# Performance work log

Hardware: AMD Instinct MI355X
Metric: run time of the kernel (lower is better)

Reference implementation:

```python
import jax, jax.numpy as jnp
import numpy as np

B = 32768
PASSES = 4

# mask layout: (batch, digit, row, col), values in {0,1}

def _to_lines(m, d):
    """Reorder so the last axis enumerates the 9 cells of a line and axis -2 the 9 lines."""
    if d == 'h':
        return m                      # lines = rows, cells = cols
    if d == 'v':
        return jnp.swapaxes(m, 2, 3)  # lines = cols, cells = rows
    b = m.shape[0]                    # lines = 3x3 boxes
    return m.reshape(b, 9, 3, 3, 3, 3).transpose(0, 1, 2, 4, 3, 5).reshape(b, 9, 9, 9)

_from_lines = _to_lines  # all three reorderings are self-inverse


def filter_line(m, d):
    """SudokuFilterHVBox: remove a solved cell's digit from all other cells in its line."""
    l = _to_lines(m, d)
    cnt = l.sum(axis=1, keepdims=True)                 # candidates per cell
    solved = l * (cnt == 1).astype(l.dtype)            # one-hot solved cells
    other = solved.sum(axis=-1, keepdims=True) - solved  # same digit solved elsewhere in line
    out = l * (other == 0).astype(l.dtype)
    return _from_lines(out, d)


def unique_line(m, d):
    """SudokuUniqueHVBox (hidden single): if a digit fits only one cell in a line, fix it."""
    l = _to_lines(m, d)
    cnt_line = l.sum(axis=-1, keepdims=True)           # per-digit count in the line
    hidden = l * (cnt_line == 1).astype(l.dtype)       # lone placements
    has = hidden.sum(axis=1, keepdims=True) > 0        # cell hosts a hidden single
    out = jnp.where(has, hidden, l)
    return _from_lines(out, d)


def doubles_line(m, d):
    """SudokuDigitsDoubles (naked pair): two identical 2-candidate cells in a line
    eliminate those digits from the rest of the line."""
    l = _to_lines(m, d)                                # (B, d, line, cell)
    cnt = l.sum(axis=1, keepdims=True)
    pm = l * (cnt == 2).astype(l.dtype)                # patterns of 2-candidate cells
    dot = jnp.einsum('bdlc,bdle->blce', pm, pm)        # pattern overlap between cells
    eye = jnp.eye(9, dtype=l.dtype)
    match = (dot == 2).astype(l.dtype) * (1.0 - eye)   # identical pair at another cell
    pairflag = match.sum(-1) > 0                       # (B, line, cell) part of a naked pair
    pair_digit = pm * pairflag[:, None, :, :].astype(l.dtype)
    total_pd = pair_digit.sum(-1, keepdims=True)       # digit belongs to some pair in line
    remove = (total_pd > 0) & (pair_digit == 0)
    out = l * (1.0 - remove.astype(l.dtype))
    return _from_lines(out, d)


def pointing(m, d):
    """SudokuDigitsInOneLineAtBox: if a digit's box candidates lie in one row/col,
    remove that digit from the rest of the row/col outside the box."""
    b = m.shape[0]
    v = m.reshape(b, 9, 3, 3, 3, 3)                    # (B, d, br, ri, bc, ci)
    if d == 'h':
        pres = v.sum(axis=5) > 0                       # (B,d,br,ri,bc) digit in row of box
        nrows = pres.sum(axis=3, keepdims=True)
        point = pres & (nrows == 1)                    # confined to single row within box
        tot = point.sum(axis=4, keepdims=True)         # over bc
        rem = (tot - point) > 0                        # pointing from another box hits us
        out = v * (1.0 - rem[..., None].astype(v.dtype))
    else:
        pres = v.sum(axis=3) > 0                       # (B,d,br,bc,ci) digit in col of box
        ncols = pres.sum(axis=4, keepdims=True)
        point = pres & (ncols == 1)
        tot = point.sum(axis=2, keepdims=True)         # over br
        rem = (tot - point) > 0
        out = v * (1.0 - rem[:, :, :, None, :, :].astype(v.dtype))
    return out.reshape(b, 9, 9, 9)


def _forward_mask(mask):
    for _ in range(PASSES):
        mask = filter_line(mask, 'box')
        mask = pointing(mask, 'h')
        mask = pointing(mask, 'v')
        mask = unique_line(mask, 'h')
        mask = unique_line(mask, 'v')
        mask = unique_line(mask, 'box')
        mask = doubles_line(mask, 'v')   # original code instantiates doubles_h with 'v'
        mask = doubles_line(mask, 'v')
        mask = doubles_line(mask, 'box')
    return mask


def setup_inputs() -> dict:
    key = jax.random.key(0)
    mask = jax.random.randint(key, (B, 9, 9, 9), 0, 2).astype(jnp.float32)
    return {"mask": mask}


def reference(mask):
    out = _forward_mask(mask)
    cnt = out.sum(axis=1)                              # candidates per cell
    solved = jnp.all(cnt == 1, axis=(1, 2))            # (B,) puzzle fully determined
    return (out, solved)
```

## Files before the change

kernel.cpp:

```cpp
#include <hip/hip_runtime.h>
#include <stdint.h>

#define NB 32768
#define NPASS 4
#define FULL27 0x07FFFFFFu
#define NBF (NB * 729)
#define PPW 20
#define NBLK ((NB + PPW - 1) / PPW)


__device__ __forceinline__ uint32_t colfold(uint32_t w) {
    return (w | (w >> 9) | (w >> 18)) & 0x1FFu;
}
__device__ __forceinline__ uint32_t colmaj2(uint32_t w) {
    return ((w & (w >> 9)) | ((w | (w >> 9)) & (w >> 18))) & 0x1FFu;
}

__global__ __launch_bounds__(64)
void sudoku_kernel(const uint32_t* __restrict__ in, float* __restrict__ out,
                   float* __restrict__ solved) {
    __shared__ uint32_t pool[460];
    const int lane = threadIdx.x;
    const int trip = lane / 3;
    const int band = lane - trip * 3;
    const int bo1 = band == 2 ? 0 : band + 1;
    const int bo2 = band == 0 ? 2 : band - 1;
    int sl1 = trip * 3 + bo1; if (sl1 > 63) sl1 = 63;
    int sl2 = trip * 3 + bo2; if (sl2 > 63) sl2 = 63;
    const int p0 = blockIdx.x * PPW;
    const int p = p0 + trip;
    const bool valid = (trip < PPW) && (p < NB);

    {
        const int base = p0 * 729;
        #pragma unroll 1
        for (int c = 0; c < 14; ++c) {
            uint32_t v[16];
            #pragma unroll
            for (int j = 0; j < 16; ++j) {
                int gi = base + (c * 16 + j) * 64 + lane;
                if (gi >= NBF) gi = NBF - 1;
                v[j] = in[gi];
            }
            #pragma unroll
            for (int j = 0; j < 16; ++j) {
                unsigned long long m = __ballot(v[j] != 0u);
                if (lane == 0) {
                    int r = c * 16 + j;
                    pool[2 * r]     = (uint32_t)m;
                    pool[2 * r + 1] = (uint32_t)(m >> 32);
                }
            }
        }
        {
            uint32_t v[4];
            #pragma unroll
            for (int j = 0; j < 4; ++j) {
                int gi = base + (224 + j) * 64 + lane;
                if (gi >= NBF) gi = NBF - 1;
                v[j] = in[gi];
            }
            #pragma unroll
            for (int j = 0; j < 4; ++j) {
                unsigned long long m = __ballot(v[j] != 0u);
                if (lane == 0) {
                    int r = 224 + j;
                    pool[2 * r]     = (uint32_t)m;
                    pool[2 * r + 1] = (uint32_t)(m >> 32);
                }
            }
        }
    }
    __syncthreads();

    uint32_t bd[9];
    {
        const int tx = trip >= PPW ? PPW - 1 : trip;
        const int bb0 = tx * 729 + band * 27;
        #pragma unroll
        for (int d = 0; d < 9; ++d) {
            int bb = bb0 + d * 81;
            int di = bb >> 5, sh = bb & 31;
            uint64_t both = (uint64_t)pool[di] | ((uint64_t)pool[di + 1] << 32);
            bd[d] = (uint32_t)(both >> sh) & FULL27;
        }
    }
    __syncthreads();

    #pragma unroll 1
    for (int pass = 0; pass < NPASS; ++pass) {
        {
            uint32_t on = 0, tw = 0, fo = 0;
            #pragma unroll
            for (int d = 0; d < 9; ++d) {
                uint32_t c = on & bd[d];
                on ^= bd[d]; fo |= tw & c; tw ^= c;
            }
            uint32_t ex1 = on & ~tw & ~fo;
            #pragma unroll
            for (int d = 0; d < 9; ++d) {
                uint32_t s = bd[d] & ex1;
                #pragma unroll
                for (int k = 0; k < 3; ++k) {
                    uint32_t bm = 0x1C0E07u << (3 * k);
                    uint32_t sm = s & bm;
                    uint32_t multi = sm & (sm - 1u);
                    uint32_t keep = (sm == 0u) ? 0xFFFFFFFFu : (~bm | (multi ? 0u : sm));
                    bd[d] &= keep;
                }
            }
        }

        #pragma unroll
        for (int d = 0; d < 9; ++d) {
            uint32_t w = bd[d];
            uint32_t t = (w | (w >> 1) | (w >> 2)) & 0x01249249u;
            uint32_t sum = (t & 0x1FFu) + ((t >> 9) & 0x1FFu) + ((t >> 18) & 0x1FFu);
            uint32_t single = sum & ~(sum >> 1) & 0x49u;
            uint32_t point = t & (single * 0x40201u);
            uint32_t clearm = 0;
            #pragma unroll
            for (int r = 0; r < 3; ++r) {
                uint32_t pr = (point >> (9 * r)) & 0x1FFu;
                uint32_t multi = pr & (pr - 1u);
                uint32_t segkeep = multi ? 0u : pr * 7u;
                uint32_t rc = pr ? ((0x1FFu & ~segkeep) << (9 * r)) : 0u;
                clearm |= rc;
            }
            bd[d] = w & ~clearm;
        }

        {
            uint32_t pnt[9];
            #pragma unroll
            for (int d = 0; d < 9; ++d) {
                uint32_t w = bd[d];
                uint32_t q = colfold(w);
                uint32_t u = (q & 0x49u) + ((q >> 1) & 0x49u) + ((q >> 2) & 0x49u);
                uint32_t single = u & ~(u >> 1) & 0x49u;
                pnt[d] = q & (single * 7u);
            }
            #pragma unroll
            for (int d = 0; d < 9; ++d) {
                uint32_t o = (uint32_t)__shfl((int)pnt[d], sl1, 64) |
                             (uint32_t)__shfl((int)pnt[d], sl2, 64);
                bd[d] &= ~(o * 0x40201u);
            }
        }

        {
            uint32_t hid[9], has = 0;
            #pragma unroll
            for (int d = 0; d < 9; ++d) {
                uint32_t w = bd[d], h = 0;
                #pragma unroll
                for (int r = 0; r < 3; ++r) {
                    uint32_t x = w & (0x1FFu << (9 * r));
                    h |= (x & (x - 1u)) ? 0u : x;
                }
                hid[d] = h; has |= h;
            }
            #pragma unroll
            for (int d = 0; d < 9; ++d) bd[d] = (bd[d] & ~has) | hid[d];
        }

        {
            uint32_t hid[9], has = 0;
            #pragma unroll
            for (int d = 0; d < 9; ++d) {
                uint32_t w = bd[d];
                uint32_t q0 = colfold(w), m0 = colmaj2(w);
                uint32_t ex = q0 | (m0 << 9);
                uint32_t ea = (uint32_t)__shfl((int)ex, sl1, 64);
                uint32_t eb = (uint32_t)__shfl((int)ex, sl2, 64);
                uint32_t qa = ea & 0x1FFu, ma = ea >> 9;
                uint32_t qb = eb & 0x1FFu, mb = eb >> 9;
                uint32_t ge2 = m0 | ma | mb | (q0 & qa) | (q0 & qb) | (qa & qb);
                uint32_t ex1c = (q0 | qa | qb) & ~ge2;
                hid[d] = w & ((ex1c & q0) * 0x40201u);
                has |= hid[d];
            }
            #pragma unroll
            for (int d = 0; d < 9; ++d) bd[d] = (bd[d] & ~has) | hid[d];
        }

        {
            uint32_t hid[9], has = 0;
            #pragma unroll
            for (int d = 0; d < 9; ++d) {
                uint32_t w = bd[d], h = 0;
                #pragma unroll
                for (int k = 0; k < 3; ++k) {
                    uint32_t x = w & (0x1C0E07u << (3 * k));
                    h |= (x & (x - 1u)) ? 0u : x;
                }
                hid[d] = h; has |= h;
            }
            #pragma unroll
            for (int d = 0; d < 9; ++d) bd[d] = (bd[d] & ~has) | hid[d];
        }

        #pragma unroll 1
        for (int rep = 0; rep < 2; ++rep) {
            uint32_t on = 0, tw = 0, fo = 0;
            #pragma unroll
            for (int d = 0; d < 9; ++d) {
                uint32_t c = on & bd[d];
                on ^= bd[d]; fo |= tw & c; tw ^= c;
            }
            uint32_t ex2 = tw & ~on & ~fo;
            uint32_t Q[9], K[9];
            #pragma unroll
            for (int d = 0; d < 9; ++d) { Q[d] = bd[d] & ex2; K[d] = 0u; }
            #pragma unroll
            for (int d1 = 0; d1 < 9; ++d1)
                #pragma unroll
                for (int d2 = d1 + 1; d2 < 9; ++d2) {
                    uint32_t P = Q[d1] & Q[d2];
                    uint32_t f0 = colfold(P), g0 = colmaj2(P);
                    uint32_t ex = f0 | (g0 << 9);
                    uint32_t ea = (uint32_t)__shfl((int)ex, sl1, 64);
                    uint32_t eb = (uint32_t)__shfl((int)ex, sl2, 64);
                    uint32_t fa = ea & 0x1FFu, ga = ea >> 9;
                    uint32_t fb = eb & 0x1FFu, gb = eb >> 9;
                    uint32_t dup = g0 | ga | gb | (f0 & fa) | (f0 & fb) | (fa & fb);
                    uint32_t sK = P & (dup * 0x40201u);
                    K[d1] |= sK; K[d2] |= sK;
                }
            #pragma unroll
            for (int d = 0; d < 9; ++d) {
                uint32_t kc = colfold(K[d]);
                uint32_t cols = kc | (uint32_t)__shfl((int)kc, sl1, 64)
                                   | (uint32_t)__shfl((int)kc, sl2, 64);
                uint32_t em = cols * 0x40201u;
                bd[d] = (bd[d] & ~em) | K[d];
            }
        }

        {
            uint32_t on = 0, tw = 0, fo = 0;
            #pragma unroll
            for (int d = 0; d < 9; ++d) {
                uint32_t c = on & bd[d];
                on ^= bd[d]; fo |= tw & c; tw ^= c;
            }
            uint32_t ex2 = tw & ~on & ~fo;
            uint32_t Q[9], K[9];
            #pragma unroll
            for (int d = 0; d < 9; ++d) { Q[d] = bd[d] & ex2; K[d] = 0u; }
            #pragma unroll
            for (int d1 = 0; d1 < 9; ++d1)
                #pragma unroll
                for (int d2 = d1 + 1; d2 < 9; ++d2) {
                    uint32_t P = Q[d1] & Q[d2];
                    #pragma unroll
                    for (int k = 0; k < 3; ++k) {
                        uint32_t m = P & (0x1C0E07u << (3 * k));
                        uint32_t s = (m & (m - 1u)) ? m : 0u;
                        K[d1] |= s; K[d2] |= s;
                    }
                }
            #pragma unroll
            for (int d = 0; d < 9; ++d)
                #pragma unroll
                for (int k = 0; k < 3; ++k) {
                    uint32_t bm = 0x1C0E07u << (3 * k);
                    uint32_t t = K[d] & bm;
                    uint32_t mask = t ? (~bm | t) : 0xFFFFFFFFu;
                    bd[d] &= mask;
                }
        }
    }

    {
        uint32_t on = 0, tw = 0, fo = 0;
        #pragma unroll
        for (int d = 0; d < 9; ++d) {
            uint32_t c = on & bd[d];
            on ^= bd[d]; fo |= tw & c; tw ^= c;
        }
        uint32_t okb = ((on & ~tw & ~fo) == FULL27) ? 1u : 0u;
        uint32_t all = okb & (uint32_t)__shfl((int)okb, sl1, 64)
                           & (uint32_t)__shfl((int)okb, sl2, 64);
        if (valid && band == 0) solved[p] = all ? 1.0f : 0.0f;
    }

    for (int j = lane; j < 456; j += 64) pool[j] = 0u;
    __syncthreads();
    if (valid) {
        const int pbit = trip * 729;
        #pragma unroll
        for (int d = 0; d < 9; ++d) {
            int bitbase = pbit + d * 81 + band * 27;
            int di = bitbase >> 5;
            int sh = bitbase & 31;
            uint64_t both = (uint64_t)bd[d] << sh;
            atomicOr(&pool[di], (uint32_t)both);
            atomicOr(&pool[di + 1], (uint32_t)(both >> 32));
        }
    }
    __syncthreads();
    {
        int nv = NB - p0; if (nv > PPW) nv = PPW;
        const int limit4 = nv * 729 / 4;
        float4* dst4 = (float4*)(out + (size_t)p0 * 729);
        #pragma unroll 4
        for (int i = 0; i < 57; ++i) {
            int j = i * 64 + lane;
            if (j < limit4) {
                uint32_t nib = (pool[j >> 3] >> ((j & 7) * 4)) & 0xFu;
                dst4[j] = make_float4((float)(nib & 1u), (float)((nib >> 1) & 1u),
                                      (float)((nib >> 2) & 1u), (float)((nib >> 3) & 1u));
            }
        }
    }
}

extern "C" void kernel_launch(void* const* d_in, const int* in_sizes, int n_in,
                              void* d_out, int out_size, void* d_ws, size_t ws_size,
                              hipStream_t stream) {
    const uint32_t* in = (const uint32_t*)d_in[0];
    float* out = (float*)d_out;
    float* solved = out + (size_t)NB * 729;
    sudoku_kernel<<<NBLK, 64, 0, stream>>>(in, out, solved);
}
```

Measured before the change: 217.0 us.

## Map each puzzle to a lane quad and swap shuffles for DPP quad permutes

Each puzzle now gets four lanes (three active bands plus one idle lane) instead of three, so each wave holds 16 puzzles rather than 20. The cross-band exchanges between the three bands of a puzzle now use DPP quad_perm rotations instead of __shfl. This removes the LDS-backed bpermute traffic from the many exchanges inside the naked-pair loops and drops the bounds and validity checks. The cost is a quarter of lanes idle and more blocks in total, so each puzzle takes more lane-time.

```diff
diff --git a/kernel.cpp b/kernel.cpp
--- a/kernel.cpp
+++ b/kernel.cpp
@@ -5,8 +5,10 @@
 #define NPASS 4
 #define FULL27 0x07FFFFFFu
 #define NBF (NB * 729)
-#define PPW 20
-#define NBLK ((NB + PPW - 1) / PPW)
+#define PPW 16
+#define NBLK (NB / PPW)
+#define ROUNDS 183
+#define POOLDW 368
 
 
 __device__ __forceinline__ uint32_t colfold(uint32_t w) {
@@ -14,27 +16,28 @@
 }
 __device__ __forceinline__ uint32_t colmaj2(uint32_t w) {
     return ((w & (w >> 9)) | ((w | (w >> 9)) & (w >> 18))) & 0x1FFu;
+}
+__device__ __forceinline__ uint32_t rotA(uint32_t v) {
+    return (uint32_t)__builtin_amdgcn_update_dpp(0, (int)v, 0x09, 0xF, 0xF, true);
+}
+__device__ __forceinline__ uint32_t rotB(uint32_t v) {
+    return (uint32_t)__builtin_amdgcn_update_dpp(0, (int)v, 0x12, 0xF, 0xF, true);
 }
 
 __global__ __launch_bounds__(64)
 void sudoku_kernel(const uint32_t* __restrict__ in, float* __restrict__ out,
                    float* __restrict__ solved) {
-    __shared__ uint32_t pool[460];
+    __shared__ uint32_t pool[POOLDW];
     const int lane = threadIdx.x;
-    const int trip = lane / 3;
-    const int band = lane - trip * 3;
-    const int bo1 = band == 2 ? 0 : band + 1;
-    const int bo2 = band == 0 ? 2 : band - 1;
-    int sl1 = trip * 3 + bo1; if (sl1 > 63) sl1 = 63;
-    int sl2 = trip * 3 + bo2; if (sl2 > 63) sl2 = 63;
+    const int trip = lane >> 2;
+    const int band = lane & 3;
     const int p0 = blockIdx.x * PPW;
     const int p = p0 + trip;
-    const bool valid = (trip < PPW) && (p < NB);
 
     {
         const int base = p0 * 729;
         #pragma unroll 1
-        for (int c = 0; c < 14; ++c) {
+        for (int c = 0; c < 11; ++c) {
             uint32_t v[16];
             #pragma unroll
             for (int j = 0; j < 16; ++j) {
@@ -53,18 +56,18 @@
             }
         }
         {
-            uint32_t v[4];
-            #pragma unroll
-            for (int j = 0; j < 4; ++j) {
-                int gi = base + (224 + j) * 64 + lane;
+            uint32_t v[7];
+            #pragma unroll
+            for (int j = 0; j < 7; ++j) {
+                int gi = base + (176 + j) * 64 + lane;
                 if (gi >= NBF) gi = NBF - 1;
                 v[j] = in[gi];
             }
             #pragma unroll
-            for (int j = 0; j < 4; ++j) {
+            for (int j = 0; j < 7; ++j) {
                 unsigned long long m = __ballot(v[j] != 0u);
                 if (lane == 0) {
-                    int r = 224 + j;
+                    int r = 176 + j;
                     pool[2 * r]     = (uint32_t)m;
                     pool[2 * r + 1] = (uint32_t)(m >> 32);
                 }
@@ -75,8 +78,7 @@
 
     uint32_t bd[9];
     {
-        const int tx = trip >= PPW ? PPW - 1 : trip;
-        const int bb0 = tx * 729 + band * 27;
+        const int bb0 = trip * 729 + band * 27;
         #pragma unroll
         for (int d = 0; d < 9; ++d) {
             int bb = bb0 + d * 81;
@@ -142,8 +144,7 @@
             }
             #pragma unroll
             for (int d = 0; d < 9; ++d) {
-                uint32_t o = (uint32_t)__shfl((int)pnt[d], sl1, 64) |
-                             (uint32_t)__shfl((int)pnt[d], sl2, 64);
+                uint32_t o = rotA(pnt[d]) | rotB(pnt[d]);
                 bd[d] &= ~(o * 0x40201u);
             }
         }
@@ -171,8 +172,8 @@
                 uint32_t w = bd[d];
                 uint32_t q0 = colfold(w), m0 = colmaj2(w);
                 uint32_t ex = q0 | (m0 << 9);
-                uint32_t ea = (uint32_t)__shfl((int)ex, sl1, 64);
-                uint32_t eb = (uint32_t)__shfl((int)ex, sl2, 64);
+                uint32_t ea = rotA(ex);
+                uint32_t eb = rotB(ex);
                 uint32_t qa = ea & 0x1FFu, ma = ea >> 9;
                 uint32_t qb = eb & 0x1FFu, mb = eb >> 9;
                 uint32_t ge2 = m0 | ma | mb | (q0 & qa) | (q0 & qb) | (qa & qb);
@@ -219,8 +220,8 @@
                     uint32_t P = Q[d1] & Q[d2];
                     uint32_t f0 = colfold(P), g0 = colmaj2(P);
                     uint32_t ex = f0 | (g0 << 9);
-                    uint32_t ea = (uint32_t)__shfl((int)ex, sl1, 64);
-                    uint32_t eb = (uint32_t)__shfl((int)ex, sl2, 64);
+                    uint32_t ea = rotA(ex);
+                    uint32_t eb = rotB(ex);
                     uint32_t fa = ea & 0x1FFu, ga = ea >> 9;
                     uint32_t fb = eb & 0x1FFu, gb = eb >> 9;
                     uint32_t dup = g0 | ga | gb | (f0 & fa) | (f0 & fb) | (fa & fb);
@@ -230,8 +231,7 @@
             #pragma unroll
             for (int d = 0; d < 9; ++d) {
                 uint32_t kc = colfold(K[d]);
-                uint32_t cols = kc | (uint32_t)__shfl((int)kc, sl1, 64)
-                                   | (uint32_t)__shfl((int)kc, sl2, 64);
+                uint32_t cols = kc | rotA(kc) | rotB(kc);
                 uint32_t em = cols * 0x40201u;
                 bd[d] = (bd[d] & ~em) | K[d];
             }
@@ -280,14 +280,13 @@
             on ^= bd[d]; fo |= tw & c; tw ^= c;
         }
         uint32_t okb = ((on & ~tw & ~fo) == FULL27) ? 1u : 0u;
-        uint32_t all = okb & (uint32_t)__shfl((int)okb, sl1, 64)
-                           & (uint32_t)__shfl((int)okb, sl2, 64);
-        if (valid && band == 0) solved[p] = all ? 1.0f : 0.0f;
-    }
-
-    for (int j = lane; j < 456; j += 64) pool[j] = 0u;
+        uint32_t all = okb & rotA(okb) & rotB(okb);
+        if (band == 0) solved[p] = all ? 1.0f : 0.0f;
+    }
+
+    for (int j = lane; j < POOLDW; j += 64) pool[j] = 0u;
     __syncthreads();
-    if (valid) {
+    if (band != 3) {
         const int pbit = trip * 729;
         #pragma unroll
         for (int d = 0; d < 9; ++d) {
@@ -301,11 +300,10 @@
     }
     __syncthreads();
     {
-        int nv = NB - p0; if (nv > PPW) nv = PPW;
-        const int limit4 = nv * 729 / 4;
+        const int limit4 = PPW * 729 / 4;
         float4* dst4 = (float4*)(out + (size_t)p0 * 729);
         #pragma unroll 4
-        for (int i = 0; i < 57; ++i) {
+        for (int i = 0; i < 46; ++i) {
             int j = i * 64 + lane;
             if (j < limit4) {
                 uint32_t nib = (pool[j >> 3] >> ((j & 7) * 4)) & 0xFu;
```

Result: no change. 213.5 us (-1.6%).
